# Performance work log

Hardware: AMD Instinct MI355X
Metric: run time of the kernel (lower is better)

The kernel has to match this reference:

```python
import jax, jax.numpy as jnp
import numpy as np

NUM_EMBEDDINGS = 1024
EMBEDDING_DIM = 64
COMMITMENT_COST = 0.25


def setup_inputs() -> dict:
    key = jax.random.key(0)
    k_in, k_cb = jax.random.split(key)
    inputs = jax.random.normal(k_in, (32, 4096, EMBEDDING_DIM), dtype=jnp.float32)
    # matches reset_embeddings(): uniform(-1/num_embeddings, 1/num_embeddings)
    bound = 1.0 / NUM_EMBEDDINGS
    codebook = jax.random.uniform(k_cb, (NUM_EMBEDDINGS, EMBEDDING_DIM),
                                  dtype=jnp.float32, minval=-bound, maxval=bound)
    return {"inputs": inputs, "codebook": codebook}


def reference(inputs, codebook):
    input_shape = inputs.shape
    D = codebook.shape[1]
    x = inputs.reshape(-1, D)  # [N, D]
    # Squared euclidean distances; argmin is invariant to the sqrt used by torch.cdist.
    # dist2[n,k] = ||x_n||^2 - 2 x_n . e_k + ||e_k||^2
    dist2 = (jnp.sum(x * x, axis=1, keepdims=True)
             - 2.0 * (x @ codebook.T)
             + jnp.sum(codebook * codebook, axis=1))  # [N, K]
    encoding_indices = jnp.argmin(dist2, axis=1)  # [N]
    quantized = codebook[encoding_indices].reshape(input_shape)
    loss = (jnp.mean((jax.lax.stop_gradient(quantized) - inputs) ** 2)
            + COMMITMENT_COST * jnp.mean((quantized - jax.lax.stop_gradient(inputs)) ** 2))
    # straight-through estimator
    quantized_st = inputs + jax.lax.stop_gradient(quantized - inputs)
    return quantized_st, loss
```

## Files before the change

kernel.cpp:

```cpp
#include <hip/hip_runtime.h>


typedef __attribute__((ext_vector_type(8))) short short8;
typedef __attribute__((ext_vector_type(4))) float f32x4;

#define VQ_D 64
#define MTILE 512
#define NTH 512
#define CSTRIDE 68

__device__ inline unsigned short f2bf(float f) {
  union { float f; unsigned u; } v; v.f = f;
  unsigned r = v.u + 0x7FFFu + ((v.u >> 16) & 1u);
  return (unsigned short)(r >> 16);
}

__global__ __launch_bounds__(256) void vq_prep(const float* __restrict__ cb,
                                               float* __restrict__ c2b,
                                               unsigned short* __restrict__ cbb,
                                               float* __restrict__ sse,
                                               unsigned* __restrict__ counter, int K) {
  if (blockIdx.x == 0 && threadIdx.x == 0) { *sse = 0.f; *counter = 0u; }
  int w = (int)((blockIdx.x * 256 + threadIdx.x) >> 6);
  int lane = threadIdx.x & 63;
  if (w >= K) return;
  float v = cb[(size_t)w * VQ_D + lane];
  cbb[(size_t)w * CSTRIDE + lane] = f2bf(v);
  if (lane < CSTRIDE - VQ_D) cbb[(size_t)w * CSTRIDE + VQ_D + lane] = 0;
  float s = v * v;
#pragma unroll
  for (int off = 32; off; off >>= 1) s += __shfl_down(s, off);
  if (lane == 0) c2b[w] = s + 0.5f;
}

__global__ __launch_bounds__(NTH) void vq_argmin(
    const float* __restrict__ x, const float* __restrict__ c2b,
    const unsigned short* __restrict__ cbb, int* __restrict__ gidx,
    float* __restrict__ out, float* __restrict__ sse_out,
    unsigned* __restrict__ counter, int nblocks) {
  __shared__ unsigned short cbs[1024 * CSTRIDE];
  __shared__ float c2s[1024];
  __shared__ int idxs[MTILE];
  __shared__ float xn[MTILE];
  __shared__ float redbuf[8];

  const int tid = threadIdx.x;
  const int wave = tid >> 6;
  const int lane = tid & 63;
  const int quad = lane >> 4;
  const int col = lane & 15;
  const long blockRow0 = (long)blockIdx.x * MTILE;
  const int waveRow0 = wave * 64;

  const char* gbase = (const char*)cbb;
#pragma unroll
  for (int i = 0; i < 17; ++i) {
    const int chunk0 = i * NTH + wave * 64;
    const char* src = gbase + (size_t)(chunk0 + lane) * 16;
    __builtin_amdgcn_global_load_lds(
        (const __attribute__((address_space(1))) void*)src,
        (__attribute__((address_space(3))) void*)(cbs + (size_t)chunk0 * 8),
        16, 0, 0);
  }
  c2s[tid] = c2b[tid];
  c2s[tid + 512] = c2b[tid + 512];

  short8 Af[4][2];
#pragma unroll
  for (int mi = 0; mi < 4; ++mi) {
    float nrm = 0.f;
#pragma unroll
    for (int ks = 0; ks < 2; ++ks) {
      long row = blockRow0 + waveRow0 + mi * 16 + col;
      const f32x4* xp = (const f32x4*)(x + row * VQ_D + ks * 32 + quad * 8);
      f32x4 lo = xp[0];
      f32x4 hi = xp[1];
      nrm += lo[0] * lo[0] + lo[1] * lo[1] + lo[2] * lo[2] + lo[3] * lo[3];
      nrm += hi[0] * hi[0] + hi[1] * hi[1] + hi[2] * hi[2] + hi[3] * hi[3];
      short8 a;
      a[0] = (short)f2bf(-2.f * lo[0]); a[1] = (short)f2bf(-2.f * lo[1]);
      a[2] = (short)f2bf(-2.f * lo[2]); a[3] = (short)f2bf(-2.f * lo[3]);
      a[4] = (short)f2bf(-2.f * hi[0]); a[5] = (short)f2bf(-2.f * hi[1]);
      a[6] = (short)f2bf(-2.f * hi[2]); a[7] = (short)f2bf(-2.f * hi[3]);
      Af[mi][ks] = a;
    }
    nrm += __shfl_xor(nrm, 16);
    nrm += __shfl_xor(nrm, 32);
    if (quad == 0) xn[waveRow0 + mi * 16 + col] = nrm;
  }

  unsigned bk[4][4];
#pragma unroll
  for (int mi = 0; mi < 4; ++mi)
#pragma unroll
    for (int r = 0; r < 4; ++r) bk[mi][r] = 0xFFFFFFFFu;

  __syncthreads();

  const unsigned short* bbase = cbs + (size_t)col * CSTRIDE + quad * 8;
#pragma unroll 4
  for (int t = 0; t < 64; ++t) {
    const unsigned short* bp = bbase + t * 16 * CSTRIDE;
    short8 b0 = *(const short8*)bp;
    short8 b1 = *(const short8*)(bp + 32);
    float cc = c2s[t * 16 + col];

    f32x4 acc[4];
#pragma unroll
    for (int mi = 0; mi < 4; ++mi) {
      f32x4 a = {cc, cc, cc, cc};
      a = __builtin_amdgcn_mfma_f32_16x16x32_bf16(Af[mi][0], b0, a, 0, 0, 0);
      a = __builtin_amdgcn_mfma_f32_16x16x32_bf16(Af[mi][1], b1, a, 0, 0, 0);
      acc[mi] = a;
    }

    const unsigned code = (unsigned)((t << 4) + col);
#pragma unroll
    for (int mi = 0; mi < 4; ++mi)
#pragma unroll
      for (int r = 0; r < 4; ++r)
        bk[mi][r] = min(bk[mi][r], (__float_as_uint(acc[mi][r]) & 0xFFFFFC00u) | code);
  }

#pragma unroll
  for (int off = 1; off < 16; off <<= 1) {
#pragma unroll
    for (int mi = 0; mi < 4; ++mi)
#pragma unroll
      for (int r = 0; r < 4; ++r) {
        unsigned o = (unsigned)__shfl_xor((int)bk[mi][r], off);
        bk[mi][r] = min(bk[mi][r], o);
      }
  }

  float sse = 0.f;
  if (col == 0) {
#pragma unroll
    for (int mi = 0; mi < 4; ++mi)
#pragma unroll
      for (int r = 0; r < 4; ++r) {
        const int row = waveRow0 + mi * 16 + quad * 4 + r;
        idxs[row] = (int)(bk[mi][r] & 1023u);
        const float s_rec = __uint_as_float(bk[mi][r] & 0xFFFFFC00u);
        sse += s_rec - 0.5f + xn[row];
      }
  }
  sse += __shfl_xor(sse, 16);
  sse += __shfl_xor(sse, 32);
  if (lane == 0) redbuf[wave] = sse;
  __syncthreads();

  gidx[blockRow0 + tid] = idxs[tid];

  if (tid == 0) {
    float s = 0.f;
#pragma unroll
    for (int w = 0; w < 8; ++w) s += redbuf[w];
    atomicAdd(sse_out, s);
    __threadfence();
    unsigned old = atomicAdd(counter, 1u);
    if (old == (unsigned)(nblocks - 1)) {
      float tot = atomicAdd(sse_out, 0.f);
      long nelem = (long)nblocks * MTILE * VQ_D;
      out[nelem] = 1.25f * tot / (float)nelem;
    }
  }
}

__global__ __launch_bounds__(256) void vq_gather(const float* __restrict__ cb,
                                                 const int* __restrict__ gidx,
                                                 float* __restrict__ out) {
  const int t = blockIdx.x * 256 + threadIdx.x;
  const f32x4* cb4 = (const f32x4*)cb;
  f32x4* out4 = (f32x4*)out;
#pragma unroll
  for (int i = 0; i < 4; ++i) {
    const int f = t + i * (1 << 19);
    const int row = f >> 4;
    const int d4 = f & 15;
    out4[f] = cb4[(size_t)gidx[row] * 16 + d4];
  }
}

extern "C" void kernel_launch(void* const* d_in, const int* in_sizes, int n_in,
                              void* d_out, int out_size, void* d_ws, size_t ws_size,
                              hipStream_t stream) {
  const float* x = (const float*)d_in[0];
  const float* cb = (const float*)d_in[1];
  float* out = (float*)d_out;

  const long n_elem = (long)in_sizes[0];
  const int nrows = (int)(n_elem / VQ_D);
  const int K = in_sizes[1] / VQ_D;
  const int nblocks = nrows / MTILE;

  char* ws = (char*)d_ws;
  float* sse = (float*)ws;
  unsigned* counter = (unsigned*)(ws + 64);
  float* c2b = (float*)(ws + 256);
  unsigned short* cbb = (unsigned short*)(ws + 8192);
  int* gidx = (int*)(ws + 8192 + 139264);

  vq_prep<<<dim3((K * 64 + 255) / 256), dim3(256), 0, stream>>>(cb, c2b, cbb, sse, counter, K);
  vq_argmin<<<dim3(nblocks), dim3(NTH), 0, stream>>>(x, c2b, cbb, gidx, out, sse, counter, nblocks);
  vq_gather<<<dim3(nrows * 16 / (256 * 4)), dim3(256), 0, stream>>>(cb, gidx, out);
}
```

Before: 129.0 us.

## Split codebook across two wave halves with 1024-thread blocks and LDS atomicMin merge

Doubles the block to 1024 threads so each row group is handled by two waves, each scanning half of the codebook (512 codes), then merges the per-row packed distance/index keys with shared-memory atomicMin. The per-wave MFMA loop is halved, raising the number of waves that can hide latency within the single block the large LDS codebook allows per CU. The cost is that both halves load and convert the same input rows, plus an extra barrier and LDS atomics. Codebook staging into LDS is redistributed over more threads with a bounds guard.

```diff
diff --git a/kernel.cpp b/kernel.cpp
--- a/kernel.cpp
+++ b/kernel.cpp
@@ -6,8 +6,9 @@
 
 #define VQ_D 64
 #define MTILE 512
-#define NTH 512
+#define NTH 1024
 #define CSTRIDE 68
+#define CHUNKS 8704
 
 __device__ inline unsigned short f2bf(float f) {
   union { float f; unsigned u; } v; v.f = f;
@@ -40,7 +41,7 @@
     unsigned* __restrict__ counter, int nblocks) {
   __shared__ unsigned short cbs[1024 * CSTRIDE];
   __shared__ float c2s[1024];
-  __shared__ int idxs[MTILE];
+  __shared__ unsigned keys[MTILE];
   __shared__ float xn[MTILE];
   __shared__ float redbuf[8];
 
@@ -49,21 +50,24 @@
   const int lane = tid & 63;
   const int quad = lane >> 4;
   const int col = lane & 15;
+  const int rg = wave & 7;
+  const int half = wave >> 3;
   const long blockRow0 = (long)blockIdx.x * MTILE;
-  const int waveRow0 = wave * 64;
 
   const char* gbase = (const char*)cbb;
 #pragma unroll
-  for (int i = 0; i < 17; ++i) {
+  for (int i = 0; i < 9; ++i) {
     const int chunk0 = i * NTH + wave * 64;
-    const char* src = gbase + (size_t)(chunk0 + lane) * 16;
-    __builtin_amdgcn_global_load_lds(
-        (const __attribute__((address_space(1))) void*)src,
-        (__attribute__((address_space(3))) void*)(cbs + (size_t)chunk0 * 8),
-        16, 0, 0);
+    if (chunk0 < CHUNKS) {
+      const char* src = gbase + (size_t)(chunk0 + lane) * 16;
+      __builtin_amdgcn_global_load_lds(
+          (const __attribute__((address_space(1))) void*)src,
+          (__attribute__((address_space(3))) void*)(cbs + (size_t)chunk0 * 8),
+          16, 0, 0);
+    }
   }
   c2s[tid] = c2b[tid];
-  c2s[tid + 512] = c2b[tid + 512];
+  if (tid < MTILE) keys[tid] = 0xFFFFFFFFu;
 
   short8 Af[4][2];
 #pragma unroll
@@ -71,12 +75,14 @@
     float nrm = 0.f;
 #pragma unroll
     for (int ks = 0; ks < 2; ++ks) {
-      long row = blockRow0 + waveRow0 + mi * 16 + col;
+      long row = blockRow0 + rg * 64 + mi * 16 + col;
       const f32x4* xp = (const f32x4*)(x + row * VQ_D + ks * 32 + quad * 8);
       f32x4 lo = xp[0];
       f32x4 hi = xp[1];
-      nrm += lo[0] * lo[0] + lo[1] * lo[1] + lo[2] * lo[2] + lo[3] * lo[3];
-      nrm += hi[0] * hi[0] + hi[1] * hi[1] + hi[2] * hi[2] + hi[3] * hi[3];
+      if (half == 0) {
+        nrm += lo[0] * lo[0] + lo[1] * lo[1] + lo[2] * lo[2] + lo[3] * lo[3];
+        nrm += hi[0] * hi[0] + hi[1] * hi[1] + hi[2] * hi[2] + hi[3] * hi[3];
+      }
       short8 a;
       a[0] = (short)f2bf(-2.f * lo[0]); a[1] = (short)f2bf(-2.f * lo[1]);
       a[2] = (short)f2bf(-2.f * lo[2]); a[3] = (short)f2bf(-2.f * lo[3]);
@@ -84,9 +90,11 @@
       a[6] = (short)f2bf(-2.f * hi[2]); a[7] = (short)f2bf(-2.f * hi[3]);
       Af[mi][ks] = a;
     }
-    nrm += __shfl_xor(nrm, 16);
-    nrm += __shfl_xor(nrm, 32);
-    if (quad == 0) xn[waveRow0 + mi * 16 + col] = nrm;
+    if (half == 0) {
+      nrm += __shfl_xor(nrm, 16);
+      nrm += __shfl_xor(nrm, 32);
+      if (quad == 0) xn[rg * 64 + mi * 16 + col] = nrm;
+    }
   }
 
   unsigned bk[4][4];
@@ -97,13 +105,13 @@
 
   __syncthreads();
 
-  const unsigned short* bbase = cbs + (size_t)col * CSTRIDE + quad * 8;
+  const unsigned short* bbase = cbs + (size_t)(half * 512 + col) * CSTRIDE + quad * 8;
 #pragma unroll 4
-  for (int t = 0; t < 64; ++t) {
+  for (int t = 0; t < 32; ++t) {
     const unsigned short* bp = bbase + t * 16 * CSTRIDE;
     short8 b0 = *(const short8*)bp;
     short8 b1 = *(const short8*)(bp + 32);
-    float cc = c2s[t * 16 + col];
+    float cc = c2s[half * 512 + t * 16 + col];
 
     f32x4 acc[4];
 #pragma unroll
@@ -114,7 +122,7 @@
       acc[mi] = a;
     }
 
-    const unsigned code = (unsigned)((t << 4) + col);
+    const unsigned code = (unsigned)(half * 512 + (t << 4) + col);
 #pragma unroll
     for (int mi = 0; mi < 4; ++mi)
 #pragma unroll
@@ -132,25 +140,26 @@
         bk[mi][r] = min(bk[mi][r], o);
       }
   }
+  if (col == 0) {
+#pragma unroll
+    for (int mi = 0; mi < 4; ++mi)
+#pragma unroll
+      for (int r = 0; r < 4; ++r)
+        atomicMin(&keys[rg * 64 + mi * 16 + quad * 4 + r], bk[mi][r]);
+  }
+  __syncthreads();
 
   float sse = 0.f;
-  if (col == 0) {
-#pragma unroll
-    for (int mi = 0; mi < 4; ++mi)
-#pragma unroll
-      for (int r = 0; r < 4; ++r) {
-        const int row = waveRow0 + mi * 16 + quad * 4 + r;
-        idxs[row] = (int)(bk[mi][r] & 1023u);
-        const float s_rec = __uint_as_float(bk[mi][r] & 0xFFFFFC00u);
-        sse += s_rec - 0.5f + xn[row];
-      }
-  }
-  sse += __shfl_xor(sse, 16);
-  sse += __shfl_xor(sse, 32);
-  if (lane == 0) redbuf[wave] = sse;
+  if (tid < MTILE) {
+    const unsigned k = keys[tid];
+    gidx[blockRow0 + tid] = (int)(k & 1023u);
+    const float s_rec = __uint_as_float(k & 0xFFFFFC00u);
+    sse = s_rec - 0.5f + xn[tid];
+#pragma unroll
+    for (int off = 32; off; off >>= 1) sse += __shfl_down(sse, off);
+    if (lane == 0) redbuf[wave] = sse;
+  }
   __syncthreads();
-
-  gidx[blockRow0 + tid] = idxs[tid];
 
   if (tid == 0) {
     float s = 0.f;
```

Result: slower. 133.8 us (+3.7%).

## Stream bf16 codebook from global with 32x32 MFMA instead of LDS staging

Applied to the files above, without the earlier changes.

The argmin kernel no longer stages the bf16 codebook and norms in LDS. Each wave now covers 32 rows and reads codebook fragments straight from global/L2 with a double-buffered register prefetch, feeding 32x32x16 bf16 MFMAs. Blocks grow to 1024 threads, and rows write their index and loss directly without shared-memory staging. The gather kernel batches its index and codebook loads before issuing nontemporal stores. This removes the large per-block LDS fill and its barrier, in exchange for repeated global codebook reads and more register pressure per wave.

```diff
diff --git a/kernel.cpp b/kernel.cpp
--- a/kernel.cpp
+++ b/kernel.cpp
@@ -3,11 +3,11 @@
 
 typedef __attribute__((ext_vector_type(8))) short short8;
 typedef __attribute__((ext_vector_type(4))) float f32x4;
+typedef __attribute__((ext_vector_type(16))) float f32x16;
 
 #define VQ_D 64
 #define MTILE 512
-#define NTH 512
-#define CSTRIDE 68
+#define NTH 1024
 
 __device__ inline unsigned short f2bf(float f) {
   union { float f; unsigned u; } v; v.f = f;
@@ -25,137 +25,110 @@
   int lane = threadIdx.x & 63;
   if (w >= K) return;
   float v = cb[(size_t)w * VQ_D + lane];
-  cbb[(size_t)w * CSTRIDE + lane] = f2bf(v);
-  if (lane < CSTRIDE - VQ_D) cbb[(size_t)w * CSTRIDE + VQ_D + lane] = 0;
+  cbb[(size_t)w * VQ_D + lane] = f2bf(v);
   float s = v * v;
 #pragma unroll
   for (int off = 32; off; off >>= 1) s += __shfl_down(s, off);
   if (lane == 0) c2b[w] = s + 0.5f;
 }
 
+#define LOADB(B, CCV, N)                                                   \
+  {                                                                        \
+    const int n_ = (N);                                                    \
+    _Pragma("unroll") for (int s_ = 0; s_ < 4; ++s_)                       \
+        B[s_] = bp8[((size_t)(n_ * 32 + c) << 3) + 2 * s_ + h];            \
+    CCV = c2b[n_ * 32 + c];                                                \
+  }
+
+#define COMPUTE(B, CCV, N)                                                 \
+  {                                                                        \
+    f32x16 a;                                                              \
+    _Pragma("unroll") for (int r_ = 0; r_ < 16; ++r_) a[r_] = CCV;         \
+    _Pragma("unroll") for (int s_ = 0; s_ < 4; ++s_)                       \
+        a = __builtin_amdgcn_mfma_f32_32x32x16_bf16(Af[s_], B[s_], a, 0, 0, 0); \
+    const unsigned code_ = (unsigned)((N)*32 + c);                         \
+    _Pragma("unroll") for (int r_ = 0; r_ < 16; ++r_)                      \
+        bk[r_] = min(bk[r_], (__float_as_uint(a[r_]) & 0xFFFFFC00u) | code_); \
+  }
+
 __global__ __launch_bounds__(NTH) void vq_argmin(
     const float* __restrict__ x, const float* __restrict__ c2b,
     const unsigned short* __restrict__ cbb, int* __restrict__ gidx,
     float* __restrict__ out, float* __restrict__ sse_out,
     unsigned* __restrict__ counter, int nblocks) {
-  __shared__ unsigned short cbs[1024 * CSTRIDE];
-  __shared__ float c2s[1024];
-  __shared__ int idxs[MTILE];
-  __shared__ float xn[MTILE];
-  __shared__ float redbuf[8];
+  __shared__ float redbuf[16];
 
   const int tid = threadIdx.x;
   const int wave = tid >> 6;
   const int lane = tid & 63;
-  const int quad = lane >> 4;
-  const int col = lane & 15;
-  const long blockRow0 = (long)blockIdx.x * MTILE;
-  const int waveRow0 = wave * 64;
+  const int c = lane & 31;
+  const int h = lane >> 5;
+  const long row0 = (long)blockIdx.x * MTILE + wave * 32;
 
-  const char* gbase = (const char*)cbb;
+  short8 Af[4];
+  float nrm = 0.f;
 #pragma unroll
-  for (int i = 0; i < 17; ++i) {
-    const int chunk0 = i * NTH + wave * 64;
-    const char* src = gbase + (size_t)(chunk0 + lane) * 16;
-    __builtin_amdgcn_global_load_lds(
-        (const __attribute__((address_space(1))) void*)src,
-        (__attribute__((address_space(3))) void*)(cbs + (size_t)chunk0 * 8),
-        16, 0, 0);
+  for (int s = 0; s < 4; ++s) {
+    const f32x4* xp = (const f32x4*)(x + (row0 + c) * VQ_D + 16 * s + 8 * h);
+    f32x4 lo = xp[0];
+    f32x4 hi = xp[1];
+    nrm += lo[0] * lo[0] + lo[1] * lo[1] + lo[2] * lo[2] + lo[3] * lo[3];
+    nrm += hi[0] * hi[0] + hi[1] * hi[1] + hi[2] * hi[2] + hi[3] * hi[3];
+    short8 a;
+    a[0] = (short)f2bf(-2.f * lo[0]); a[1] = (short)f2bf(-2.f * lo[1]);
+    a[2] = (short)f2bf(-2.f * lo[2]); a[3] = (short)f2bf(-2.f * lo[3]);
+    a[4] = (short)f2bf(-2.f * hi[0]); a[5] = (short)f2bf(-2.f * hi[1]);
+    a[6] = (short)f2bf(-2.f * hi[2]); a[7] = (short)f2bf(-2.f * hi[3]);
+    Af[s] = a;
   }
-  c2s[tid] = c2b[tid];
-  c2s[tid + 512] = c2b[tid + 512];
+  nrm += __shfl_xor(nrm, 32);
 
-  short8 Af[4][2];
+  unsigned bk[16];
 #pragma unroll
-  for (int mi = 0; mi < 4; ++mi) {
-    float nrm = 0.f;
-#pragma unroll
-    for (int ks = 0; ks < 2; ++ks) {
-      long row = blockRow0 + waveRow0 + mi * 16 + col;
-      const f32x4* xp = (const f32x4*)(x + row * VQ_D + ks * 32 + quad * 8);
-      f32x4 lo = xp[0];
-      f32x4 hi = xp[1];
-      nrm += lo[0] * lo[0] + lo[1] * lo[1] + lo[2] * lo[2] + lo[3] * lo[3];
-      nrm += hi[0] * hi[0] + hi[1] * hi[1] + hi[2] * hi[2] + hi[3] * hi[3];
-      short8 a;
-      a[0] = (short)f2bf(-2.f * lo[0]); a[1] = (short)f2bf(-2.f * lo[1]);
-      a[2] = (short)f2bf(-2.f * lo[2]); a[3] = (short)f2bf(-2.f * lo[3]);
-      a[4] = (short)f2bf(-2.f * hi[0]); a[5] = (short)f2bf(-2.f * hi[1]);
-      a[6] = (short)f2bf(-2.f * hi[2]); a[7] = (short)f2bf(-2.f * hi[3]);
-      Af[mi][ks] = a;
-    }
-    nrm += __shfl_xor(nrm, 16);
-    nrm += __shfl_xor(nrm, 32);
-    if (quad == 0) xn[waveRow0 + mi * 16 + col] = nrm;
-  }
+  for (int r = 0; r < 16; ++r) bk[r] = 0xFFFFFFFFu;
 
-  unsigned bk[4][4];
-#pragma unroll
-  for (int mi = 0; mi < 4; ++mi)
-#pragma unroll
-    for (int r = 0; r < 4; ++r) bk[mi][r] = 0xFFFFFFFFu;
-
-  __syncthreads();
-
-  const unsigned short* bbase = cbs + (size_t)col * CSTRIDE + quad * 8;
-#pragma unroll 4
-  for (int t = 0; t < 64; ++t) {
-    const unsigned short* bp = bbase + t * 16 * CSTRIDE;
-    short8 b0 = *(const short8*)bp;
-    short8 b1 = *(const short8*)(bp + 32);
-    float cc = c2s[t * 16 + col];
-
-    f32x4 acc[4];
-#pragma unroll
-    for (int mi = 0; mi < 4; ++mi) {
-      f32x4 a = {cc, cc, cc, cc};
-      a = __builtin_amdgcn_mfma_f32_16x16x32_bf16(Af[mi][0], b0, a, 0, 0, 0);
-      a = __builtin_amdgcn_mfma_f32_16x16x32_bf16(Af[mi][1], b1, a, 0, 0, 0);
-      acc[mi] = a;
-    }
-
-    const unsigned code = (unsigned)((t << 4) + col);
-#pragma unroll
-    for (int mi = 0; mi < 4; ++mi)
-#pragma unroll
-      for (int r = 0; r < 4; ++r)
-        bk[mi][r] = min(bk[mi][r], (__float_as_uint(acc[mi][r]) & 0xFFFFFC00u) | code);
+  const short8* bp8 = (const short8*)cbb;
+  short8 B0[4], B1[4];
+  float cc0, cc1;
+  LOADB(B0, cc0, 0);
+#pragma unroll 2
+  for (int n = 0; n < 32; n += 2) {
+    LOADB(B1, cc1, n + 1);
+    COMPUTE(B0, cc0, n);
+    if (n + 2 < 32) LOADB(B0, cc0, n + 2);
+    COMPUTE(B1, cc1, n + 1);
   }
 
 #pragma unroll
-  for (int off = 1; off < 16; off <<= 1) {
+  for (int off = 1; off < 32; off <<= 1) {
 #pragma unroll
-    for (int mi = 0; mi < 4; ++mi)
-#pragma unroll
-      for (int r = 0; r < 4; ++r) {
-        unsigned o = (unsigned)__shfl_xor((int)bk[mi][r], off);
-        bk[mi][r] = min(bk[mi][r], o);
-      }
+    for (int r = 0; r < 16; ++r) {
+      unsigned o = (unsigned)__shfl_xor((int)bk[r], off);
+      bk[r] = min(bk[r], o);
+    }
   }
 
+  const int myreg = (c & 3) + 4 * (c >> 3);
+  unsigned mykey = 0xFFFFFFFFu;
+#pragma unroll
+  for (int r = 0; r < 16; ++r)
+    if (r == myreg) mykey = bk[r];
+
   float sse = 0.f;
-  if (col == 0) {
+  if (((c >> 2) & 1) == h) {
+    gidx[row0 + c] = (int)(mykey & 1023u);
+    const float s_rec = __uint_as_float(mykey & 0xFFFFFC00u);
+    sse = s_rec - 0.5f + nrm;
+  }
 #pragma unroll
-    for (int mi = 0; mi < 4; ++mi)
-#pragma unroll
-      for (int r = 0; r < 4; ++r) {
-        const int row = waveRow0 + mi * 16 + quad * 4 + r;
-        idxs[row] = (int)(bk[mi][r] & 1023u);
-        const float s_rec = __uint_as_float(bk[mi][r] & 0xFFFFFC00u);
-        sse += s_rec - 0.5f + xn[row];
-      }
-  }
-  sse += __shfl_xor(sse, 16);
-  sse += __shfl_xor(sse, 32);
+  for (int off = 32; off; off >>= 1) sse += __shfl_down(sse, off);
   if (lane == 0) redbuf[wave] = sse;
   __syncthreads();
-
-  gidx[blockRow0 + tid] = idxs[tid];
 
   if (tid == 0) {
     float s = 0.f;
 #pragma unroll
-    for (int w = 0; w < 8; ++w) s += redbuf[w];
+    for (int w = 0; w < 16; ++w) s += redbuf[w];
     atomicAdd(sse_out, s);
     __threadfence();
     unsigned old = atomicAdd(counter, 1u);
@@ -173,13 +146,18 @@
   const int t = blockIdx.x * 256 + threadIdx.x;
   const f32x4* cb4 = (const f32x4*)cb;
   f32x4* out4 = (f32x4*)out;
+  int idx[4];
+#pragma unroll
+  for (int i = 0; i < 4; ++i) idx[i] = gidx[(t + i * (1 << 19)) >> 4];
+  f32x4 cv[4];
 #pragma unroll
   for (int i = 0; i < 4; ++i) {
-    const int f = t + i * (1 << 19);
-    const int row = f >> 4;
-    const int d4 = f & 15;
-    out4[f] = cb4[(size_t)gidx[row] * 16 + d4];
+    const int d4 = (t + i * (1 << 19)) & 15;
+    cv[i] = cb4[(size_t)idx[i] * 16 + d4];
   }
+#pragma unroll
+  for (int i = 0; i < 4; ++i)
+    __builtin_nontemporal_store(cv[i], &out4[t + i * (1 << 19)]);
 }
 
 extern "C" void kernel_launch(void* const* d_in, const int* in_sizes, int n_in,
```

Measured after the change: 172.1 us. 33.4% more time.
